# Performance work log

Hardware: AMD Instinct MI355X
Metric: run time of the kernel (lower is better)

## Reference

```python
import jax, jax.numpy as jnp
import numpy as np

NEG_SLOPE = 0.2

def gat_conv(x, edge, W, att_src, att_dst, bias, heads, out_ch, concat):
    # x: [N, F_in], edge: [2, E] (self-loops already included)
    N = x.shape[0]
    src, dst = edge[0], edge[1]
    h = (x @ W).reshape(N, heads, out_ch)                     # [N, H, C]
    a_src = jnp.sum(h * att_src, axis=-1)                     # [N, H]
    a_dst = jnp.sum(h * att_dst, axis=-1)                     # [N, H]
    e = jax.nn.leaky_relu(a_src[src] + a_dst[dst], NEG_SLOPE)  # [E, H]
    # segment softmax over incoming edges of each dst node
    e_max = jax.ops.segment_max(e, dst, num_segments=N)       # [N, H]
    e_exp = jnp.exp(e - e_max[dst])                           # [E, H]
    denom = jax.ops.segment_sum(e_exp, dst, num_segments=N)   # [N, H]
    alpha = e_exp / denom[dst]                                # [E, H]
    msg = h[src] * alpha[:, :, None]                          # [E, H, C]
    out = jax.ops.segment_sum(msg, dst, num_segments=N)       # [N, H, C]
    if concat:
        out = out.reshape(N, heads * out_ch)
    else:
        out = out.mean(axis=1)
    return out + bias


def setup_inputs() -> dict:
    key = jax.random.key(0)
    ks = jax.random.split(key, 10)
    N, E = 50000, 1600000
    F_in, H, C1, n_cls = 256, 4, 64, 40
    x = jax.random.normal(ks[0], (N, F_in), dtype=jnp.float32)
    edge_index = jax.random.randint(ks[1], (2, E), 0, N, dtype=jnp.int64)
    s1 = 1.0 / np.sqrt(F_in)
    s2 = 1.0 / np.sqrt(H * C1)
    return {
        "x": x,
        "edge_index": edge_index,
        "W1": jax.random.normal(ks[2], (F_in, H * C1), dtype=jnp.float32) * s1,
        "att_src1": jax.random.normal(ks[3], (H, C1), dtype=jnp.float32) * s2,
        "att_dst1": jax.random.normal(ks[4], (H, C1), dtype=jnp.float32) * s2,
        "b1": jnp.zeros((H * C1,), dtype=jnp.float32),
        "W2": jax.random.normal(ks[5], (H * C1, n_cls), dtype=jnp.float32) * s2,
        "att_src2": jax.random.normal(ks[6], (1, n_cls), dtype=jnp.float32) * 0.1,
        "att_dst2": jax.random.normal(ks[7], (1, n_cls), dtype=jnp.float32) * 0.1,
        "b2": jnp.zeros((n_cls,), dtype=jnp.float32),
    }


def reference(x, edge_index, W1, att_src1, att_dst1, b1, W2, att_src2, att_dst2, b2):
    N = x.shape[0]
    # PyG GATConv adds self-loops by default
    loops = jnp.arange(N, dtype=edge_index.dtype)
    edge = jnp.concatenate([edge_index, jnp.stack([loops, loops])], axis=1)
    # dropout is identity in eval mode
    h = gat_conv(x, edge, W1, att_src1, att_dst1, b1, heads=4, out_ch=64, concat=True)
    h = jax.nn.elu(h)
    out = gat_conv(h, edge, W2, att_src2, att_dst2, b2, heads=1, out_ch=40, concat=False)
    return out
```

## Files before the change

kernel.cpp:

```cpp
#include <hip/hip_runtime.h>
#include <hip/hip_bf16.h>

typedef short bf16x8 __attribute__((ext_vector_type(8)));
typedef float f32x4 __attribute__((ext_vector_type(4)));
typedef float f32x2 __attribute__((ext_vector_type(2)));
typedef unsigned short u16x8 __attribute__((ext_vector_type(8)));

#define CHUNK 4096
#define BCAP 16384

__device__ __forceinline__ float wred_sum(float v) {
  #pragma unroll
  for (int off = 32; off > 0; off >>= 1)
    v += __shfl_xor(v, off, 64);
  return v;
}
__device__ __forceinline__ float b2f(unsigned short u) {
  union { unsigned int i; float f; } x;
  x.i = ((unsigned int)u) << 16;
  return x.f;
}
__device__ __forceinline__ unsigned short f2bu(float f) {
  __hip_bfloat16 b = __float2bfloat16(f);
  return *(unsigned short*)&b;
}
__device__ __forceinline__ void pkfma(f32x2& acc, f32x2 v, f32x2 w) {
  asm("v_pk_fma_f32 %0, %1, %2, %0" : "+v"(acc) : "v"(v), "v"(w));
}
__device__ __forceinline__ void qfma(f32x2* acc2, unsigned int u, f32x2 wp) {
  f32x2 a, b;
  a[0] = (float)(u & 0xFFu);         a[1] = (float)((u >> 8) & 0xFFu);
  b[0] = (float)((u >> 16) & 0xFFu); b[1] = (float)(u >> 24);
  pkfma(acc2[0], a, wp);
  pkfma(acc2[1], b, wp);
}
__device__ __forceinline__ void bffma(f32x2& acc, unsigned int up, f32x2 wp) {
  union { unsigned int i; float f; } lo, hi;
  lo.i = up << 16; hi.i = up & 0xFFFF0000u;
  f32x2 v; v[0] = lo.f; v[1] = hi.f;
  pkfma(acc, v, wp);
}
__device__ __forceinline__ float ldf(const void* p, long long i, int is16) {
  return is16 ? __bfloat162float(((const __hip_bfloat16*)p)[i])
              : ((const float*)p)[i];
}
__device__ __forceinline__ int edge_at(const int* e, long long idx, int is64) {
  return is64 ? (int)((const long long*)e)[idx] : e[idx];
}

__global__ void detect_kernel(const int* __restrict__ edge, int n_edge_check,
                              const unsigned int* __restrict__ xw, int n_x_check,
                              int* __restrict__ flag,
                              int* __restrict__ bcursor, int NB) {
  __shared__ int s_nz, s_cnt, s_tot;
  int tid = threadIdx.x;
  for (int b = tid; b < NB; b += 256) bcursor[b] = b * BCAP;
  if (tid == 0) { s_nz = 0; s_cnt = 0; s_tot = 0; }
  __syncthreads();
  int nz = 0;
  for (int k = tid; k < n_edge_check; k += 256)
    if (edge[2 * k + 1] != 0) nz = 1;
  if (nz) atomicOr(&s_nz, 1);
  int c = 0, t = 0;
  for (int k = tid; k < n_x_check; k += 256) {
    unsigned int w = xw[k];
    if (w == 0u) continue;
    t++;
    unsigned int e = (w >> 7) & 0xFFu;
    if (e >= 100u && e <= 150u) c++;
  }
  atomicAdd(&s_cnt, c);
  atomicAdd(&s_tot, t);
  __syncthreads();
  if (tid == 0) {
    flag[0] = (s_nz == 0) ? 1 : 0;
    flag[1] = (s_cnt * 10 > s_tot * 6) ? 1 : 0;
  }
}

__global__ __launch_bounds__(256) void partition_kernel(
    const int* __restrict__ edge, int E, int N, const int* __restrict__ flag,
    int* __restrict__ bcursor, unsigned int* __restrict__ part, int NB) {
  __shared__ int cnt[1024];
  __shared__ int loff[1025];
  __shared__ int gpos[1024];
  __shared__ int lcur[1024];
  __shared__ unsigned int staged[CHUNK];
  __shared__ int staged_addr[CHUNK];
  __shared__ int s[256];
  __shared__ int rbase;
  int tid = threadIdx.x;
  long long base = (long long)blockIdx.x * CHUNK;
  long long total = (long long)E + N;
  int maxa = NB * BCAP - 1;
  int here = (int)min((long long)CHUNK, total - base);
  for (int b = tid; b < NB; b += 256) cnt[b] = 0;
  if (tid == 0) rbase = 0;
  __syncthreads();
  int is64 = flag[0];
  int myb[16];
  unsigned int myp[16];
  #pragma unroll
  for (int j = 0; j < 16; j++) {
    long long i = base + j * 256 + tid;
    myb[j] = -1;
    if (i < total) {
      int d, sv;
      if (i < E) {
        sv = edge_at(edge, i, is64);
        d = edge_at(edge, (long long)E + i, is64);
      } else {
        sv = d = (int)(i - E);
      }
      d = min(max(d, 0), N - 1);
      sv = min(max(sv, 0), N - 1);
      myb[j] = d >> 8;
      myp[j] = ((unsigned int)(d & 255) << 24) | (unsigned int)sv;
      atomicAdd(&cnt[myb[j]], 1);
    }
  }
  __syncthreads();
  for (int c0 = 0; c0 < NB; c0 += 256) {
    int idx = c0 + tid;
    int v = (idx < NB) ? cnt[idx] : 0;
    s[tid] = v;
    __syncthreads();
    for (int off = 1; off < 256; off <<= 1) {
      int t = (tid >= off) ? s[tid - off] : 0;
      __syncthreads();
      s[tid] += t;
      __syncthreads();
    }
    int mb = rbase;
    if (idx < NB) loff[idx] = mb + s[tid] - v;
    __syncthreads();
    if (tid == 0) rbase = mb + s[255];
    __syncthreads();
  }
  __syncthreads();
  for (int b = tid; b < NB; b += 256) {
    int c = cnt[b];
    gpos[b] = c ? atomicAdd(&bcursor[b], c) : 0;
    lcur[b] = loff[b];
  }
  __syncthreads();
  #pragma unroll
  for (int j = 0; j < 16; j++) {
    if (myb[j] >= 0) {
      int b = myb[j];
      int slot = atomicAdd(&lcur[b], 1);
      staged[slot] = myp[j];
      staged_addr[slot] = min(gpos[b] + (slot - loff[b]), maxa);
    }
  }
  __syncthreads();
  for (int i = tid; i < here; i += 256)
    part[staged_addr[i]] = staged[i];
}

__global__ __launch_bounds__(256) void bucket_sort_kernel(
    const unsigned int* __restrict__ part, const int* __restrict__ bcursor,
    int N, int* __restrict__ indptr, int* __restrict__ iend,
    int* __restrict__ ssrc) {
  __shared__ int hist[256], cur[256];
  __shared__ int s[256];
  int tid = threadIdx.x;
  int b = blockIdx.x;
  int begin = b * BCAP, end = bcursor[b];
  hist[tid] = 0;
  __syncthreads();
  for (int i = begin + tid; i < end; i += 256)
    atomicAdd(&hist[part[i] >> 24], 1);
  __syncthreads();
  int v = hist[tid];
  s[tid] = v;
  __syncthreads();
  for (int off = 1; off < 256; off <<= 1) {
    int t = (tid >= off) ? s[tid - off] : 0;
    __syncthreads();
    s[tid] += t;
    __syncthreads();
  }
  int exc = s[tid] - v;
  cur[tid] = exc;
  int d = b * 256 + tid;
  if (d < N) { indptr[d] = begin + exc; iend[d] = begin + exc + v; }
  __syncthreads();
  for (int i = begin + tid; i < end; i += 256) {
    unsigned int p = part[i];
    int pos = begin + atomicAdd(&cur[p >> 24], 1);
    ssrc[pos] = (int)(p & 0xFFFFFFu);
  }
}

__global__ void prep_kernel(const void* __restrict__ W1v, const void* __restrict__ W2v,
                            __hip_bfloat16* __restrict__ Wt1, __hip_bfloat16* __restrict__ Wt2,
                            int F, int HC, int C2, int C2p,
                            const int* __restrict__ dflag) {
  int f16 = dflag[1];
  int i = blockIdx.x * 256 + threadIdx.x;
  int n1 = HC * F;
  if (i < n1) {
    int n = i / F, k = i - n * F;
    Wt1[i] = __float2bfloat16(ldf(W1v, (long long)k * HC + n, f16));
  } else {
    int jj = i - n1;
    if (jj >= C2p * HC) return;
    int n = jj / HC, k = jj - n * HC;
    float v = (n < C2) ? ldf(W2v, (long long)k * C2 + n, f16) : 0.f;
    Wt2[jj] = __float2bfloat16(v);
  }
}

__global__ __launch_bounds__(256) void mfma_gemm_kernel(
    const void* __restrict__ A, const __hip_bfloat16* __restrict__ BtT,
    __hip_bfloat16* __restrict__ Cb,
    const void* __restrict__ attS, const void* __restrict__ attD,
    float* __restrict__ aS, float* __restrict__ aD,
    float2* __restrict__ aSq, int NT,
    int M, int Nout, int K, int quant, int amode,
    unsigned char* __restrict__ h1q,
    const int* __restrict__ dflag) {
  int nwg = gridDim.x;
  int i0 = blockIdx.x;
  int qd = nwg >> 3, rm = nwg & 7;
  int xcd = i0 & 7, idx = i0 >> 3;
  int logical = (xcd < rm ? xcd * (qd + 1) : rm * (qd + 1) + (xcd - rm) * qd) + idx;
  int colt = logical % NT;
  int rowt = logical / NT;
  int row0 = rowt * 64, col0 = colt * 64;

  int f16 = dflag[1];
  int af16 = amode | f16;
  int tid = threadIdx.x;
  int w = tid >> 6, l = tid & 63;
  int m_lane = l & 15, q = l >> 4;
  int arow = row0 + w * 16 + m_lane;
  bool aok = (arow < M);
  const __hip_bfloat16* Ab = (const __hip_bfloat16*)A + (long long)arow * K + q * 8;
  const float* Af = (const float*)A + (long long)arow * K + q * 8;
  const __hip_bfloat16* Brow = BtT + (long long)(col0 + m_lane) * K + q * 8;
  f32x4 acc[4] = {};
  #pragma unroll 4
  for (int k0 = 0; k0 < K; k0 += 32) {
    bf16x8 af = {};
    if (aok) {
      if (af16) {
        af = *(const bf16x8*)(Ab + k0);
      } else {
        float4 u0 = *(const float4*)(Af + k0);
        float4 u1 = *(const float4*)(Af + k0 + 4);
        af[0] = (short)f2bu(u0.x); af[1] = (short)f2bu(u0.y);
        af[2] = (short)f2bu(u0.z); af[3] = (short)f2bu(u0.w);
        af[4] = (short)f2bu(u1.x); af[5] = (short)f2bu(u1.y);
        af[6] = (short)f2bu(u1.z); af[7] = (short)f2bu(u1.w);
      }
    }
    #pragma unroll
    for (int t = 0; t < 4; t++) {
      bf16x8 bf = *(const bf16x8*)(Brow + (long long)t * 16 * K + k0);
      acc[t] = __builtin_amdgcn_mfma_f32_16x16x32_bf16(af, bf, acc[t], 0, 0, 0);
    }
  }
  #pragma unroll
  for (int r = 0; r < 4; r++) {
    int gr = row0 + w * 16 + q * 4 + r;
    float ps = 0.f, pd = 0.f, vmax = 0.f;
    #pragma unroll
    for (int t = 0; t < 4; t++) {
      int gc = col0 + t * 16 + m_lane;
      float v = acc[t][r];
      if (gc < Nout) {
        ps += v * ldf(attS, gc, f16);
        pd += v * ldf(attD, gc, f16);
        vmax = fmaxf(vmax, fabsf(v));
        if (!quant && gr < M) Cb[(long long)gr * Nout + gc] = __float2bfloat16(v);
      }
    }
    #pragma unroll
    for (int off = 1; off < 16; off <<= 1) {
      ps += __shfl_xor(ps, off, 64);
      pd += __shfl_xor(pd, off, 64);
      vmax = fmaxf(vmax, __shfl_xor(vmax, off, 64));
    }
    if (quant && gr < M) {
      float qinv = (vmax > 0.f) ? 127.f / vmax : 0.f;
      #pragma unroll
      for (int t = 0; t < 4; t++) {
        int gc = col0 + t * 16 + m_lane;
        h1q[(long long)gr * 256 + gc] =
            (unsigned char)(__float2int_rn(acc[t][r] * qinv) + 128);
      }
      if (m_lane == 0) {
        float2 sq; sq.x = ps; sq.y = vmax * (1.f / 127.f);
        aSq[(long long)gr * NT + colt] = sq;
      }
    }
    if (m_lane == 0 && gr < M) {
      if (!quant) aS[(long long)gr * NT + colt] = ps;
      aD[(long long)gr * NT + colt] = pd;
    }
  }
}

__global__ __launch_bounds__(256) void aggregate1_kernel(
    const int* __restrict__ indptr, const int* __restrict__ iend,
    const int* __restrict__ ssrc,
    const unsigned char* __restrict__ h1q, const float2* __restrict__ a_sq,
    const float* __restrict__ a_dst, const void* __restrict__ b1,
    __hip_bfloat16* __restrict__ h2b, int N, const int* __restrict__ dflag) {
  int f16 = dflag[1];
  int w = threadIdx.x >> 6, l = threadIdx.x & 63;
  int d = blockIdx.x * 4 + w;
  if (d >= N) return;
  int q = l >> 4;
  int e16 = l & 15;
  int hb = (l & 12) << 2;
  int chb = (l & 15) << 4;
  int begin = indptr[d], end = iend[d];
  float adst = a_dst[d * 4 + q];
  int s0 = ssrc[begin];
  float den = 0.f, accS = 0.f;
  f32x2 acc2[8] = {};
  for (int c = begin; c < end; c += 32) {
    int cnt = end - c;
    int sj0 = s0, sj1 = s0;
    float ws0 = 0.f, ws1 = 0.f;
    if (e16 < cnt) {
      sj0 = ssrc[c + e16];
      float2 t = a_sq[sj0 * 4 + q];
      float e = t.x + adst;
      e = (e > 0.f) ? e : 0.2f * e;
      float wj = __expf(e);
      den += wj; ws0 = wj * t.y;
    }
    if (e16 + 16 < cnt) {
      sj1 = ssrc[c + 16 + e16];
      float2 t = a_sq[sj1 * 4 + q];
      float e = t.x + adst;
      e = (e > 0.f) ? e : 0.2f * e;
      float wj = __expf(e);
      den += wj; ws1 = wj * t.y;
    }
    int m0 = cnt < 16 ? cnt : 16;
    int m1 = cnt - 16; m1 = m1 < 0 ? 0 : (m1 > 16 ? 16 : m1);
    int j0 = (m0 + 3) >> 2, j1 = (m1 + 3) >> 2;
    #pragma unroll 4
    for (int j = 0; j < j0; j++) {
      int idx = hb + 4 * j + q;
      int s = __shfl(sj0, idx, 64);
      float wt = __shfl(ws0, idx, 64);
      accS += wt;
      f32x2 wp; wp[0] = wt; wp[1] = wt;
      uint4 uv = *(const uint4*)(h1q + (long long)s * 256 + chb);
      qfma(&acc2[0], uv.x, wp);
      qfma(&acc2[2], uv.y, wp);
      qfma(&acc2[4], uv.z, wp);
      qfma(&acc2[6], uv.w, wp);
    }
    #pragma unroll 4
    for (int j = 0; j < j1; j++) {
      int idx = hb + 4 * j + q;
      int s = __shfl(sj1, idx, 64);
      float wt = __shfl(ws1, idx, 64);
      accS += wt;
      f32x2 wp; wp[0] = wt; wp[1] = wt;
      uint4 uv = *(const uint4*)(h1q + (long long)s * 256 + chb);
      qfma(&acc2[0], uv.x, wp);
      qfma(&acc2[2], uv.y, wp);
      qfma(&acc2[4], uv.z, wp);
      qfma(&acc2[6], uv.w, wp);
    }
  }
  float* af = (float*)acc2;
  #pragma unroll
  for (int i = 0; i < 16; i++) {
    af[i] += __shfl_xor(af[i], 16, 64);
    af[i] += __shfl_xor(af[i], 32, 64);
  }
  accS += __shfl_xor(accS, 16, 64);
  accS += __shfl_xor(accS, 32, 64);
  #pragma unroll
  for (int off = 1; off < 16; off <<= 1)
    den += __shfl_xor(den, off, 64);
  float deh = __shfl(den, hb, 64);
  float inv = 1.f / deh;
  if (l < 16) {
    u16x8 o0, o1;
    #pragma unroll
    for (int i = 0; i < 16; i++) {
      float v = (af[i] - 128.f * accS) * inv + ldf(b1, chb + i, f16);
      v = (v > 0.f) ? v : (__expf(v) - 1.f);
      if (i < 8) o0[i] = f2bu(v); else o1[i - 8] = f2bu(v);
    }
    u16x8* dst = (u16x8*)((unsigned short*)h2b + (long long)d * 256 + chb);
    dst[0] = o0;
    dst[1] = o1;
  }
}

__global__ __launch_bounds__(256) void aggregate2_kernel(
    const int* __restrict__ indptr, const int* __restrict__ iend,
    const int* __restrict__ ssrc,
    const __hip_bfloat16* __restrict__ gb, const float* __restrict__ a_src,
    const float* __restrict__ a_dst, const void* __restrict__ b2,
    void* __restrict__ out, int N, int C, const int* __restrict__ dflag) {
  int f16 = dflag[1];
  int w = threadIdx.x >> 6, l = threadIdx.x & 63;
  int d = blockIdx.x * 4 + w;
  if (d >= N) return;
  int begin = indptr[d], end = iend[d];
  float adst = a_dst[d];
  int eg = l / 10;
  int cq = l - eg * 10;
  bool act = (eg < 6);
  int s0 = ssrc[begin];
  float den = 0.f;
  f32x2 acc01 = {0.f, 0.f}, acc23 = {0.f, 0.f};
  for (int c = begin; c < end; c += 64) {
    int cnt = min(64, end - c);
    int sj = s0;
    float wj = 0.f;
    if (l < cnt) {
      sj = ssrc[c + l];
      float e = a_src[sj] + adst;
      e = (e > 0.f) ? e : 0.2f * e;
      wj = __expf(e);
    }
    den += wj;
    int jm = (cnt + 5) / 6;
    #pragma unroll 4
    for (int j = 0; j < jm; j++) {
      int idx = 6 * j + eg;
      int s = __shfl(sj, idx & 63, 64);
      float wt = __shfl(wj, idx & 63, 64);
      if (!act || idx >= cnt) wt = 0.f;
      uint2 gv = *(const uint2*)((const unsigned short*)gb +
                                 (long long)s * C + 4 * cq);
      f32x2 wp; wp[0] = wt; wp[1] = wt;
      bffma(acc01, gv.x, wp);
      bffma(acc23, gv.y, wp);
    }
  }
  den = wred_sum(den);
  float inv = 1.f / den;
  float a0 = acc01[0], a1 = acc01[1], a2 = acc23[0], a3 = acc23[1];
  #pragma unroll
  for (int k = 1; k < 6; k++) {
    int srcl = cq + 10 * k;
    a0 += __shfl(acc01[0], srcl, 64);
    a1 += __shfl(acc01[1], srcl, 64);
    a2 += __shfl(acc23[0], srcl, 64);
    a3 += __shfl(acc23[1], srcl, 64);
  }
  if (l < 10) {
    float v0 = a0 * inv + ldf(b2, 4 * l + 0, f16);
    float v1 = a1 * inv + ldf(b2, 4 * l + 1, f16);
    float v2 = a2 * inv + ldf(b2, 4 * l + 2, f16);
    float v3 = a3 * inv + ldf(b2, 4 * l + 3, f16);
    long long o = (long long)d * C + 4 * l;
    if (f16) {
      ushort4 ov;
      ov.x = f2bu(v0); ov.y = f2bu(v1); ov.z = f2bu(v2); ov.w = f2bu(v3);
      *(ushort4*)((unsigned short*)out + o) = ov;
    } else {
      float4 ov;
      ov.x = v0; ov.y = v1; ov.z = v2; ov.w = v3;
      *(float4*)((float*)out + o) = ov;
    }
  }
}

extern "C" void kernel_launch(void* const* d_in, const int* in_sizes, int n_in,
                              void* d_out, int out_size, void* d_ws, size_t ws_size,
                              hipStream_t stream) {
  const void* x   = d_in[0];
  const int* edge = (const int*)d_in[1];
  const void* W1  = d_in[2];
  const void* as1 = d_in[3];
  const void* ad1 = d_in[4];
  const void* b1  = d_in[5];
  const void* W2  = d_in[6];
  const void* as2 = d_in[7];
  const void* ad2 = d_in[8];
  const void* b2  = d_in[9];

  const int F  = 256;
  const int HC = 256;
  const int N  = in_sizes[0] / F;
  const int E  = in_sizes[1] / 2;
  const int C2 = in_sizes[9];
  const int C2p = 64;
  const int total = E + N;
  const int NB = (N + 255) / 256;
  const int Mpad = ((N + 63) / 64) * 64;

  char* p = (char*)d_ws;
  auto alloc = [&](size_t bytes) -> void* {
    void* r = (void*)p;
    p += (bytes + 255) & ~(size_t)255;
    return r;
  };
  unsigned char*  h1q = (unsigned char*)alloc((size_t)Mpad * HC);
  __hip_bfloat16* h2b = (__hip_bfloat16*)alloc((size_t)Mpad * HC * 2);
  __hip_bfloat16* gb  = (__hip_bfloat16*)alloc((size_t)Mpad * C2 * 2);
  __hip_bfloat16* Wt1 = (__hip_bfloat16*)alloc((size_t)HC * F * 2);
  __hip_bfloat16* Wt2 = (__hip_bfloat16*)alloc((size_t)C2p * HC * 2);
  float2* a_sq1 = (float2*)alloc((size_t)N * 4 * 8);
  float* a_dst1 = (float*)alloc((size_t)N * 4 * 4);
  float* a_src2 = (float*)alloc((size_t)N * 4);
  float* a_dst2 = (float*)alloc((size_t)N * 4);
  unsigned int* part = (unsigned int*)alloc((size_t)NB * BCAP * 4);
  int* ssrc     = (int*)alloc((size_t)NB * BCAP * 4);
  int* bcursor  = (int*)alloc((size_t)NB * 4);
  int* indptr   = (int*)alloc((size_t)N * 4);
  int* iend     = (int*)alloc((size_t)N * 4);
  int* flag     = (int*)alloc(256);

  detect_kernel<<<1, 256, 0, stream>>>(edge, E < 2048 ? E : 2048,
                                       (const unsigned int*)x, 4096, flag,
                                       bcursor, NB);
  int nch = (total + CHUNK - 1) / CHUNK;
  partition_kernel<<<nch, 256, 0, stream>>>(edge, E, N, flag, bcursor, part, NB);
  bucket_sort_kernel<<<NB, 256, 0, stream>>>(part, bcursor, N, indptr, iend, ssrc);

  int nprep = HC * F + C2p * HC;
  prep_kernel<<<(nprep + 255) / 256, 256, 0, stream>>>(
      W1, W2, Wt1, Wt2, F, HC, C2, C2p, flag);

  mfma_gemm_kernel<<<4 * (Mpad / 64), 256, 0, stream>>>(
      x, Wt1, nullptr, as1, ad1, nullptr, a_dst1, a_sq1, 4,
      N, HC, F, 1, 0, h1q, flag);
  aggregate1_kernel<<<(N + 3) / 4, 256, 0, stream>>>(indptr, iend, ssrc, h1q, a_sq1,
                                                     a_dst1, b1, h2b, N, flag);

  mfma_gemm_kernel<<<Mpad / 64, 256, 0, stream>>>(
      h2b, Wt2, gb, as2, ad2, a_src2, a_dst2, nullptr, 1,
      N, C2, HC, 0, 1, nullptr, flag);
  aggregate2_kernel<<<(N + 3) / 4, 256, 0, stream>>>(indptr, iend, ssrc, gb, a_src2, a_dst2,
                                                     b2, d_out, N, C2, flag);
}
```

Baseline: 371.5 us.

## Fuse layer-2 linear projection and attention logits into aggregate1 epilogue

The second GEMM (h2 @ W2) moves into the end of aggregate1. After ELU, each wave broadcasts its packed bf16 hidden row through shuffles and does a 256x40 dot product per node with packed FMA against a pre-transposed W2 layout, then writes gb and the layer-2 src/dst attention scalars directly. This removes the h2b round trip through global memory and one kernel launch. In exchange the MFMA GEMM is replaced by scalar FMA work, 128 shuffles and a W2 load per node inside the aggregation kernel.

```diff
diff --git a/kernel.cpp b/kernel.cpp
--- a/kernel.cpp
+++ b/kernel.cpp
@@ -4,7 +4,6 @@
 typedef short bf16x8 __attribute__((ext_vector_type(8)));
 typedef float f32x4 __attribute__((ext_vector_type(4)));
 typedef float f32x2 __attribute__((ext_vector_type(2)));
-typedef unsigned short u16x8 __attribute__((ext_vector_type(8)));
 
 #define CHUNK 4096
 #define BCAP 16384
@@ -39,6 +38,14 @@
   lo.i = up << 16; hi.i = up & 0xFFFF0000u;
   f32x2 v; v[0] = lo.f; v[1] = hi.f;
   pkfma(acc, v, wp);
+}
+__device__ __forceinline__ void bf2fma(f32x2& acc, unsigned int hp, unsigned int wp) {
+  union { unsigned int i; float f; } hl, hh, wl, wh;
+  hl.i = hp << 16; hh.i = hp & 0xFFFF0000u;
+  wl.i = wp << 16; wh.i = wp & 0xFFFF0000u;
+  f32x2 vh; vh[0] = hl.f; vh[1] = hh.f;
+  f32x2 vw; vw[0] = wl.f; vw[1] = wh.f;
+  pkfma(acc, vh, vw);
 }
 __device__ __forceinline__ float ldf(const void* p, long long i, int is16) {
   return is16 ? __bfloat162float(((const __hip_bfloat16*)p)[i])
@@ -194,8 +201,8 @@
 }
 
 __global__ void prep_kernel(const void* __restrict__ W1v, const void* __restrict__ W2v,
-                            __hip_bfloat16* __restrict__ Wt1, __hip_bfloat16* __restrict__ Wt2,
-                            int F, int HC, int C2, int C2p,
+                            __hip_bfloat16* __restrict__ Wt1, unsigned int* __restrict__ WT2t,
+                            int F, int HC, int C2,
                             const int* __restrict__ dflag) {
   int f16 = dflag[1];
   int i = blockIdx.x * 256 + threadIdx.x;
@@ -205,20 +212,19 @@
     Wt1[i] = __float2bfloat16(ldf(W1v, (long long)k * HC + n, f16));
   } else {
     int jj = i - n1;
-    if (jj >= C2p * HC) return;
-    int n = jj / HC, k = jj - n * HC;
-    float v = (n < C2) ? ldf(W2v, (long long)k * C2 + n, f16) : 0.f;
-    Wt2[jj] = __float2bfloat16(v);
+    if (jj >= (HC / 2) * 64) return;
+    int pr = jj >> 6, c2 = jj & 63;
+    float w0 = (c2 < C2) ? ldf(W2v, (long long)(2 * pr) * C2 + c2, f16) : 0.f;
+    float w1 = (c2 < C2) ? ldf(W2v, (long long)(2 * pr + 1) * C2 + c2, f16) : 0.f;
+    WT2t[jj] = ((unsigned int)f2bu(w1) << 16) | (unsigned int)f2bu(w0);
   }
 }
 
 __global__ __launch_bounds__(256) void mfma_gemm_kernel(
     const void* __restrict__ A, const __hip_bfloat16* __restrict__ BtT,
-    __hip_bfloat16* __restrict__ Cb,
     const void* __restrict__ attS, const void* __restrict__ attD,
-    float* __restrict__ aS, float* __restrict__ aD,
-    float2* __restrict__ aSq, int NT,
-    int M, int Nout, int K, int quant, int amode,
+    float* __restrict__ aD, float2* __restrict__ aSq, int NT,
+    int M, int Nout, int K,
     unsigned char* __restrict__ h1q,
     const int* __restrict__ dflag) {
   int nwg = gridDim.x;
@@ -231,7 +237,6 @@
   int row0 = rowt * 64, col0 = colt * 64;
 
   int f16 = dflag[1];
-  int af16 = amode | f16;
   int tid = threadIdx.x;
   int w = tid >> 6, l = tid & 63;
   int m_lane = l & 15, q = l >> 4;
@@ -245,7 +250,7 @@
   for (int k0 = 0; k0 < K; k0 += 32) {
     bf16x8 af = {};
     if (aok) {
-      if (af16) {
+      if (f16) {
         af = *(const bf16x8*)(Ab + k0);
       } else {
         float4 u0 = *(const float4*)(Af + k0);
@@ -274,7 +279,6 @@
         ps += v * ldf(attS, gc, f16);
         pd += v * ldf(attD, gc, f16);
         vmax = fmaxf(vmax, fabsf(v));
-        if (!quant && gr < M) Cb[(long long)gr * Nout + gc] = __float2bfloat16(v);
       }
     }
     #pragma unroll
@@ -283,7 +287,7 @@
       pd += __shfl_xor(pd, off, 64);
       vmax = fmaxf(vmax, __shfl_xor(vmax, off, 64));
     }
-    if (quant && gr < M) {
+    if (gr < M) {
       float qinv = (vmax > 0.f) ? 127.f / vmax : 0.f;
       #pragma unroll
       for (int t = 0; t < 4; t++) {
@@ -294,11 +298,8 @@
       if (m_lane == 0) {
         float2 sq; sq.x = ps; sq.y = vmax * (1.f / 127.f);
         aSq[(long long)gr * NT + colt] = sq;
+        aD[(long long)gr * NT + colt] = pd;
       }
-    }
-    if (m_lane == 0 && gr < M) {
-      if (!quant) aS[(long long)gr * NT + colt] = ps;
-      aD[(long long)gr * NT + colt] = pd;
     }
   }
 }
@@ -308,7 +309,11 @@
     const int* __restrict__ ssrc,
     const unsigned char* __restrict__ h1q, const float2* __restrict__ a_sq,
     const float* __restrict__ a_dst, const void* __restrict__ b1,
-    __hip_bfloat16* __restrict__ h2b, int N, const int* __restrict__ dflag) {
+    const unsigned int* __restrict__ WT2t,
+    const void* __restrict__ as2, const void* __restrict__ ad2,
+    float* __restrict__ a_src2, float* __restrict__ a_dst2,
+    __hip_bfloat16* __restrict__ gb, int C2,
+    int N, const int* __restrict__ dflag) {
   int f16 = dflag[1];
   int w = threadIdx.x >> 6, l = threadIdx.x & 63;
   int d = blockIdx.x * 4 + w;
@@ -385,18 +390,30 @@
     den += __shfl_xor(den, off, 64);
   float deh = __shfl(den, hb, 64);
   float inv = 1.f / deh;
-  if (l < 16) {
-    u16x8 o0, o1;
-    #pragma unroll
-    for (int i = 0; i < 16; i++) {
-      float v = (af[i] - 128.f * accS) * inv + ldf(b1, chb + i, f16);
-      v = (v > 0.f) ? v : (__expf(v) - 1.f);
-      if (i < 8) o0[i] = f2bu(v); else o1[i - 8] = f2bu(v);
-    }
-    u16x8* dst = (u16x8*)((unsigned short*)h2b + (long long)d * 256 + chb);
-    dst[0] = o0;
-    dst[1] = o1;
-  }
+  unsigned int wv[8];
+  #pragma unroll
+  for (int i = 0; i < 8; i++) {
+    float v0 = (af[2 * i]     - 128.f * accS) * inv + ldf(b1, chb + 2 * i, f16);
+    float v1 = (af[2 * i + 1] - 128.f * accS) * inv + ldf(b1, chb + 2 * i + 1, f16);
+    v0 = (v0 > 0.f) ? v0 : (__expf(v0) - 1.f);
+    v1 = (v1 > 0.f) ? v1 : (__expf(v1) - 1.f);
+    wv[i] = ((unsigned int)f2bu(v1) << 16) | (unsigned int)f2bu(v0);
+  }
+  f32x2 gacc = {0.f, 0.f};
+  #pragma unroll 16
+  for (int p = 0; p < 128; p++) {
+    unsigned int hp = (unsigned int)__shfl((int)wv[p & 7], p >> 3, 64);
+    unsigned int wp2 = WT2t[(p << 6) + l];
+    bf2fma(gacc, hp, wp2);
+  }
+  float gbv = gacc[0] + gacc[1];
+  float ps2 = (l < C2) ? gbv * ldf(as2, l, f16) : 0.f;
+  float pd2 = (l < C2) ? gbv * ldf(ad2, l, f16) : 0.f;
+  ps2 = wred_sum(ps2);
+  pd2 = wred_sum(pd2);
+  if (l == 0) { a_src2[d] = ps2; a_dst2[d] = pd2; }
+  if (l < C2)
+    ((unsigned short*)gb)[(long long)d * C2 + l] = f2bu(gbv);
 }
 
 __global__ __launch_bounds__(256) void aggregate2_kernel(
@@ -490,7 +507,6 @@
   const int N  = in_sizes[0] / F;
   const int E  = in_sizes[1] / 2;
   const int C2 = in_sizes[9];
-  const int C2p = 64;
   const int total = E + N;
   const int NB = (N + 255) / 256;
   const int Mpad = ((N + 63) / 64) * 64;
@@ -502,10 +518,9 @@
     return r;
   };
   unsigned char*  h1q = (unsigned char*)alloc((size_t)Mpad * HC);
-  __hip_bfloat16* h2b = (__hip_bfloat16*)alloc((size_t)Mpad * HC * 2);
   __hip_bfloat16* gb  = (__hip_bfloat16*)alloc((size_t)Mpad * C2 * 2);
   __hip_bfloat16* Wt1 = (__hip_bfloat16*)alloc((size_t)HC * F * 2);
-  __hip_bfloat16* Wt2 = (__hip_bfloat16*)alloc((size_t)C2p * HC * 2);
+  unsigned int*  WT2t = (unsigned int*)alloc((size_t)(HC / 2) * 64 * 4);
   float2* a_sq1 = (float2*)alloc((size_t)N * 4 * 8);
   float* a_dst1 = (float*)alloc((size_t)N * 4 * 4);
   float* a_src2 = (float*)alloc((size_t)N * 4);
@@ -524,19 +539,17 @@
   partition_kernel<<<nch, 256, 0, stream>>>(edge, E, N, flag, bcursor, part, NB);
   bucket_sort_kernel<<<NB, 256, 0, stream>>>(part, bcursor, N, indptr, iend, ssrc);
 
-  int nprep = HC * F + C2p * HC;
+  int nprep = HC * F + (HC / 2) * 64;
   prep_kernel<<<(nprep + 255) / 256, 256, 0, stream>>>(
-      W1, W2, Wt1, Wt2, F, HC, C2, C2p, flag);
+      W1, W2, Wt1, WT2t, F, HC, C2, flag);
 
   mfma_gemm_kernel<<<4 * (Mpad / 64), 256, 0, stream>>>(
-      x, Wt1, nullptr, as1, ad1, nullptr, a_dst1, a_sq1, 4,
-      N, HC, F, 1, 0, h1q, flag);
-  aggregate1_kernel<<<(N + 3) / 4, 256, 0, stream>>>(indptr, iend, ssrc, h1q, a_sq1,
-                                                     a_dst1, b1, h2b, N, flag);
-
-  mfma_gemm_kernel<<<Mpad / 64, 256, 0, stream>>>(
-      h2b, Wt2, gb, as2, ad2, a_src2, a_dst2, nullptr, 1,
-      N, C2, HC, 0, 1, nullptr, flag);
+      x, Wt1, as1, ad1, a_dst1, a_sq1, 4, N, HC, F, h1q, flag);
+
+  aggregate1_kernel<<<(N + 3) / 4, 256, 0, stream>>>(
+      indptr, iend, ssrc, h1q, a_sq1, a_dst1, b1,
+      WT2t, as2, ad2, a_src2, a_dst2, gb, C2, N, flag);
+
   aggregate2_kernel<<<(N + 3) / 4, 256, 0, stream>>>(indptr, iend, ssrc, gb, a_src2, a_dst2,
                                                      b2, d_out, N, C2, flag);
 }
```

Measured after the change: 464.9 us. 25.1% more time.

## Merge weight prep into partition and bucket sort into layer-1 GEMM launches

Applied to the files above, without the earlier changes.

Folds the weight transpose/convert work into extra blocks of the partition kernel, and runs the bucket-sort blocks alongside the layer-1 GEMM tiles in a single launch. This cuts two kernel launches and lets independent work share the GPU instead of serializing small kernels. The GEMM kernel is split into a specialized quantized layer-1 path and a simpler layer-2 path. A side effect is that the heavy shared-memory arrays and divergent roles share one kernel, which may affect occupancy.

```diff
diff --git a/kernel.cpp b/kernel.cpp
--- a/kernel.cpp
+++ b/kernel.cpp
@@ -78,9 +78,12 @@
   }
 }
 
-__global__ __launch_bounds__(256) void partition_kernel(
+__global__ __launch_bounds__(256) void part_prep_kernel(
     const int* __restrict__ edge, int E, int N, const int* __restrict__ flag,
-    int* __restrict__ bcursor, unsigned int* __restrict__ part, int NB) {
+    int* __restrict__ bcursor, unsigned int* __restrict__ part, int NB, int nch,
+    const void* __restrict__ W1v, const void* __restrict__ W2v,
+    __hip_bfloat16* __restrict__ Wt1, __hip_bfloat16* __restrict__ Wt2,
+    int F, int HC, int C2, int C2p) {
   __shared__ int cnt[1024];
   __shared__ int loff[1025];
   __shared__ int gpos[1024];
@@ -90,6 +93,23 @@
   __shared__ int s[256];
   __shared__ int rbase;
   int tid = threadIdx.x;
+  int f16 = flag[1];
+  if (blockIdx.x >= nch) {
+    long long i = (long long)(blockIdx.x - nch) * 256 + tid;
+    int n1 = HC * F;
+    if (i < n1) {
+      int idx = (int)i;
+      int n = idx / F, k = idx - n * F;
+      Wt1[idx] = __float2bfloat16(ldf(W1v, (long long)k * HC + n, f16));
+    } else {
+      int jj = (int)(i - n1);
+      if (jj >= C2p * HC) return;
+      int n = jj / HC, k = jj - n * HC;
+      float v = (n < C2) ? ldf(W2v, (long long)k * C2 + n, f16) : 0.f;
+      Wt2[jj] = __float2bfloat16(v);
+    }
+    return;
+  }
   long long base = (long long)blockIdx.x * CHUNK;
   long long total = (long long)E + N;
   int maxa = NB * BCAP - 1;
@@ -158,71 +178,50 @@
     part[staged_addr[i]] = staged[i];
 }
 
-__global__ __launch_bounds__(256) void bucket_sort_kernel(
+__global__ __launch_bounds__(256) void bsort_gemm_kernel(
     const unsigned int* __restrict__ part, const int* __restrict__ bcursor,
     int N, int* __restrict__ indptr, int* __restrict__ iend,
-    int* __restrict__ ssrc) {
+    int* __restrict__ ssrc, int NBS,
+    const void* __restrict__ A, const __hip_bfloat16* __restrict__ BtT,
+    const void* __restrict__ attS, const void* __restrict__ attD,
+    float* __restrict__ aD, float2* __restrict__ aSq, int NT,
+    int M, int K,
+    unsigned char* __restrict__ h1q,
+    const int* __restrict__ dflag) {
   __shared__ int hist[256], cur[256];
   __shared__ int s[256];
   int tid = threadIdx.x;
-  int b = blockIdx.x;
-  int begin = b * BCAP, end = bcursor[b];
-  hist[tid] = 0;
-  __syncthreads();
-  for (int i = begin + tid; i < end; i += 256)
-    atomicAdd(&hist[part[i] >> 24], 1);
-  __syncthreads();
-  int v = hist[tid];
-  s[tid] = v;
-  __syncthreads();
-  for (int off = 1; off < 256; off <<= 1) {
-    int t = (tid >= off) ? s[tid - off] : 0;
-    __syncthreads();
-    s[tid] += t;
-    __syncthreads();
-  }
-  int exc = s[tid] - v;
-  cur[tid] = exc;
-  int d = b * 256 + tid;
-  if (d < N) { indptr[d] = begin + exc; iend[d] = begin + exc + v; }
-  __syncthreads();
-  for (int i = begin + tid; i < end; i += 256) {
-    unsigned int p = part[i];
-    int pos = begin + atomicAdd(&cur[p >> 24], 1);
-    ssrc[pos] = (int)(p & 0xFFFFFFu);
-  }
-}
-
-__global__ void prep_kernel(const void* __restrict__ W1v, const void* __restrict__ W2v,
-                            __hip_bfloat16* __restrict__ Wt1, __hip_bfloat16* __restrict__ Wt2,
-                            int F, int HC, int C2, int C2p,
-                            const int* __restrict__ dflag) {
-  int f16 = dflag[1];
-  int i = blockIdx.x * 256 + threadIdx.x;
-  int n1 = HC * F;
-  if (i < n1) {
-    int n = i / F, k = i - n * F;
-    Wt1[i] = __float2bfloat16(ldf(W1v, (long long)k * HC + n, f16));
-  } else {
-    int jj = i - n1;
-    if (jj >= C2p * HC) return;
-    int n = jj / HC, k = jj - n * HC;
-    float v = (n < C2) ? ldf(W2v, (long long)k * C2 + n, f16) : 0.f;
-    Wt2[jj] = __float2bfloat16(v);
-  }
-}
-
-__global__ __launch_bounds__(256) void mfma_gemm_kernel(
-    const void* __restrict__ A, const __hip_bfloat16* __restrict__ BtT,
-    __hip_bfloat16* __restrict__ Cb,
-    const void* __restrict__ attS, const void* __restrict__ attD,
-    float* __restrict__ aS, float* __restrict__ aD,
-    float2* __restrict__ aSq, int NT,
-    int M, int Nout, int K, int quant, int amode,
-    unsigned char* __restrict__ h1q,
-    const int* __restrict__ dflag) {
-  int nwg = gridDim.x;
-  int i0 = blockIdx.x;
+  if (blockIdx.x < NBS) {
+    int b = blockIdx.x;
+    int begin = b * BCAP, end = bcursor[b];
+    hist[tid] = 0;
+    __syncthreads();
+    for (int i = begin + tid; i < end; i += 256)
+      atomicAdd(&hist[part[i] >> 24], 1);
+    __syncthreads();
+    int v = hist[tid];
+    s[tid] = v;
+    __syncthreads();
+    for (int off = 1; off < 256; off <<= 1) {
+      int t = (tid >= off) ? s[tid - off] : 0;
+      __syncthreads();
+      s[tid] += t;
+      __syncthreads();
+    }
+    int exc = s[tid] - v;
+    cur[tid] = exc;
+    int d = b * 256 + tid;
+    if (d < N) { indptr[d] = begin + exc; iend[d] = begin + exc + v; }
+    __syncthreads();
+    for (int i = begin + tid; i < end; i += 256) {
+      unsigned int p = part[i];
+      int pos = begin + atomicAdd(&cur[p >> 24], 1);
+      ssrc[pos] = (int)(p & 0xFFFFFFu);
+    }
+    return;
+  }
+  int nwg = gridDim.x - NBS;
+  int i0 = blockIdx.x - NBS;
   int qd = nwg >> 3, rm = nwg & 7;
   int xcd = i0 & 7, idx = i0 >> 3;
   int logical = (xcd < rm ? xcd * (qd + 1) : rm * (qd + 1) + (xcd - rm) * qd) + idx;
@@ -231,8 +230,6 @@
   int row0 = rowt * 64, col0 = colt * 64;
 
   int f16 = dflag[1];
-  int af16 = amode | f16;
-  int tid = threadIdx.x;
   int w = tid >> 6, l = tid & 63;
   int m_lane = l & 15, q = l >> 4;
   int arow = row0 + w * 16 + m_lane;
@@ -245,7 +242,7 @@
   for (int k0 = 0; k0 < K; k0 += 32) {
     bf16x8 af = {};
     if (aok) {
-      if (af16) {
+      if (f16) {
         af = *(const bf16x8*)(Ab + k0);
       } else {
         float4 u0 = *(const float4*)(Af + k0);
@@ -268,14 +265,11 @@
     float ps = 0.f, pd = 0.f, vmax = 0.f;
     #pragma unroll
     for (int t = 0; t < 4; t++) {
+      float v = acc[t][r];
       int gc = col0 + t * 16 + m_lane;
-      float v = acc[t][r];
-      if (gc < Nout) {
-        ps += v * ldf(attS, gc, f16);
-        pd += v * ldf(attD, gc, f16);
-        vmax = fmaxf(vmax, fabsf(v));
-        if (!quant && gr < M) Cb[(long long)gr * Nout + gc] = __float2bfloat16(v);
-      }
+      ps += v * ldf(attS, gc, f16);
+      pd += v * ldf(attD, gc, f16);
+      vmax = fmaxf(vmax, fabsf(v));
     }
     #pragma unroll
     for (int off = 1; off < 16; off <<= 1) {
@@ -283,7 +277,7 @@
       pd += __shfl_xor(pd, off, 64);
       vmax = fmaxf(vmax, __shfl_xor(vmax, off, 64));
     }
-    if (quant && gr < M) {
+    if (gr < M) {
       float qinv = (vmax > 0.f) ? 127.f / vmax : 0.f;
       #pragma unroll
       for (int t = 0; t < 4; t++) {
@@ -294,10 +288,68 @@
       if (m_lane == 0) {
         float2 sq; sq.x = ps; sq.y = vmax * (1.f / 127.f);
         aSq[(long long)gr * NT + colt] = sq;
+        aD[(long long)gr * NT + colt] = pd;
       }
     }
+  }
+}
+
+__global__ __launch_bounds__(256) void mfma_gemm_kernel(
+    const void* __restrict__ A, const __hip_bfloat16* __restrict__ BtT,
+    __hip_bfloat16* __restrict__ Cb,
+    const void* __restrict__ attS, const void* __restrict__ attD,
+    float* __restrict__ aS, float* __restrict__ aD, int NT,
+    int M, int Nout, int K,
+    const int* __restrict__ dflag) {
+  int nwg = gridDim.x;
+  int i0 = blockIdx.x;
+  int qd = nwg >> 3, rm = nwg & 7;
+  int xcd = i0 & 7, idx = i0 >> 3;
+  int logical = (xcd < rm ? xcd * (qd + 1) : rm * (qd + 1) + (xcd - rm) * qd) + idx;
+  int colt = logical % NT;
+  int rowt = logical / NT;
+  int row0 = rowt * 64, col0 = colt * 64;
+
+  int f16 = dflag[1];
+  int tid = threadIdx.x;
+  int w = tid >> 6, l = tid & 63;
+  int m_lane = l & 15, q = l >> 4;
+  int arow = row0 + w * 16 + m_lane;
+  bool aok = (arow < M);
+  const __hip_bfloat16* Ab = (const __hip_bfloat16*)A + (long long)arow * K + q * 8;
+  const __hip_bfloat16* Brow = BtT + (long long)(col0 + m_lane) * K + q * 8;
+  f32x4 acc[4] = {};
+  #pragma unroll 4
+  for (int k0 = 0; k0 < K; k0 += 32) {
+    bf16x8 af = {};
+    if (aok) af = *(const bf16x8*)(Ab + k0);
+    #pragma unroll
+    for (int t = 0; t < 4; t++) {
+      bf16x8 bf = *(const bf16x8*)(Brow + (long long)t * 16 * K + k0);
+      acc[t] = __builtin_amdgcn_mfma_f32_16x16x32_bf16(af, bf, acc[t], 0, 0, 0);
+    }
+  }
+  #pragma unroll
+  for (int r = 0; r < 4; r++) {
+    int gr = row0 + w * 16 + q * 4 + r;
+    float ps = 0.f, pd = 0.f;
+    #pragma unroll
+    for (int t = 0; t < 4; t++) {
+      int gc = col0 + t * 16 + m_lane;
+      float v = acc[t][r];
+      if (gc < Nout) {
+        ps += v * ldf(attS, gc, f16);
+        pd += v * ldf(attD, gc, f16);
+        if (gr < M) Cb[(long long)gr * Nout + gc] = __float2bfloat16(v);
+      }
+    }
+    #pragma unroll
+    for (int off = 1; off < 16; off <<= 1) {
+      ps += __shfl_xor(ps, off, 64);
+      pd += __shfl_xor(pd, off, 64);
+    }
     if (m_lane == 0 && gr < M) {
-      if (!quant) aS[(long long)gr * NT + colt] = ps;
+      aS[(long long)gr * NT + colt] = ps;
       aD[(long long)gr * NT + colt] = pd;
     }
   }
@@ -520,23 +572,23 @@
   detect_kernel<<<1, 256, 0, stream>>>(edge, E < 2048 ? E : 2048,
                                        (const unsigned int*)x, 4096, flag,
                                        bcursor, NB);
+
   int nch = (total + CHUNK - 1) / CHUNK;
-  partition_kernel<<<nch, 256, 0, stream>>>(edge, E, N, flag, bcursor, part, NB);
-  bucket_sort_kernel<<<NB, 256, 0, stream>>>(part, bcursor, N, indptr, iend, ssrc);
-
-  int nprep = HC * F + C2p * HC;
-  prep_kernel<<<(nprep + 255) / 256, 256, 0, stream>>>(
-      W1, W2, Wt1, Wt2, F, HC, C2, C2p, flag);
-
-  mfma_gemm_kernel<<<4 * (Mpad / 64), 256, 0, stream>>>(
-      x, Wt1, nullptr, as1, ad1, nullptr, a_dst1, a_sq1, 4,
-      N, HC, F, 1, 0, h1q, flag);
+  int nprep = (HC * F + C2p * HC + 255) / 256;
+  part_prep_kernel<<<nch + nprep, 256, 0, stream>>>(
+      edge, E, N, flag, bcursor, part, NB, nch,
+      W1, W2, Wt1, Wt2, F, HC, C2, C2p);
+
+  bsort_gemm_kernel<<<NB + 4 * (Mpad / 64), 256, 0, stream>>>(
+      part, bcursor, N, indptr, iend, ssrc, NB,
+      x, Wt1, as1, ad1, a_dst1, a_sq1, 4, N, F, h1q, flag);
+
   aggregate1_kernel<<<(N + 3) / 4, 256, 0, stream>>>(indptr, iend, ssrc, h1q, a_sq1,
                                                      a_dst1, b1, h2b, N, flag);
 
   mfma_gemm_kernel<<<Mpad / 64, 256, 0, stream>>>(
-      h2b, Wt2, gb, as2, ad2, a_src2, a_dst2, nullptr, 1,
-      N, C2, HC, 0, 1, nullptr, flag);
+      h2b, Wt2, gb, as2, ad2, a_src2, a_dst2, 1,
+      N, C2, HC, flag);
   aggregate2_kernel<<<(N + 3) / 4, 256, 0, stream>>>(indptr, iend, ssrc, gb, a_src2, a_dst2,
                                                      b2, d_out, N, C2, flag);
 }
```

Result: faster. 359.5 us (-3.2%).
